# Performance work log

Measured on AMD Instinct MI355X. Metric: run time of the kernel, lower is better.

## Reference

```python
import jax, jax.numpy as jnp
import numpy as np

N_NODES = 50000
IN_F, HID_F, OUT_F = 256, 128, 40
N_EDGES = 800000


def _uniform(key, shape, scale):
    return jax.random.uniform(key, shape, dtype=jnp.float32, minval=-scale, maxval=scale)


def setup_inputs() -> dict:
    key = jax.random.key(0)
    ks = jax.random.split(key, 20)
    x = jax.random.normal(ks[0], (N_NODES, IN_F), dtype=jnp.float32)
    edge_index = jax.random.randint(ks[1], (2, N_EDGES), 0, N_NODES, dtype=jnp.int64)
    s0, sa0 = 1.0 / np.sqrt(HID_F), 1.0  # std_att = 1/sqrt(1)
    s1, sa1 = 1.0 / np.sqrt(OUT_F), 1.0
    sv = 1.0 / np.sqrt(3.0)
    return {
        "x": x, "edge_index": edge_index,
        "Wl0": _uniform(ks[2], (IN_F, HID_F), s0),
        "Wh0": _uniform(ks[3], (IN_F, HID_F), s0),
        "Wm0": _uniform(ks[4], (IN_F, HID_F), s0),
        "al0": _uniform(ks[5], (HID_F, 1), sa0),
        "ah0": _uniform(ks[6], (HID_F, 1), sa0),
        "am0": _uniform(ks[7], (HID_F, 1), sa0),
        "att0": _uniform(ks[8], (3, 3), sv),
        "Wl1": _uniform(ks[9], (HID_F, OUT_F), s1),
        "Wh1": _uniform(ks[10], (HID_F, OUT_F), s1),
        "Wm1": _uniform(ks[11], (HID_F, OUT_F), s1),
        "al1": _uniform(ks[12], (OUT_F, 1), sa1),
        "ah1": _uniform(ks[13], (OUT_F, 1), sa1),
        "am1": _uniform(ks[14], (OUT_F, 1), sa1),
        "att1": _uniform(ks[15], (3, 3), sv),
    }


def _acm_layer(x, row, col, d_inv, Wl, Wh, Wm, al, ah, am, att):
    n = x.shape[0]
    hl, hh, hm = x @ Wl, x @ Wh, x @ Wm
    # adj_low @ M  with adj_low = D^{-1}(I + A): gather sources, scatter-add to rows
    def low(M):
        return d_inv[:, None] * (M + jax.ops.segment_sum(M[col], row, num_segments=n))
    out_low = jax.nn.relu(low(hl))
    out_high = jax.nn.relu(hh - low(hh))  # adj_high = I - adj_low
    out_mlp = jax.nn.relu(hm)
    T = 3.0
    sig = jax.nn.sigmoid(jnp.concatenate([out_low @ al, out_high @ ah, out_mlp @ am], axis=1))  # [n,3]
    a = jax.nn.softmax((sig @ att) / T, axis=1)
    return 3.0 * (a[:, 0:1] * out_low + a[:, 1:2] * out_high + a[:, 2:3] * out_mlp)


def reference(x, edge_index, Wl0, Wh0, Wm0, al0, ah0, am0, att0,
              Wl1, Wh1, Wm1, al1, ah1, am1, att1):
    n = x.shape[0]
    row, col = edge_index[0], edge_index[1]
    deg = jax.ops.segment_sum(jnp.ones_like(row, dtype=jnp.float32), row, num_segments=n)
    rowsum = 1.0 + deg  # rowsum of I + A (duplicates counted, as in scipy)
    d_inv = jnp.where(rowsum > 0, 1.0 / rowsum, 0.0)
    h = _acm_layer(x, row, col, d_inv, Wl0, Wh0, Wm0, al0, ah0, am0, att0)
    out = _acm_layer(h, row, col, d_inv, Wl1, Wh1, Wm1, al1, ah1, am1, att1)
    return out
```

## Files before the change

kernel.cpp:

```cpp
#include <hip/hip_runtime.h>
#include <math.h>

#define N_NODES 50000
#define N_EDGES 800000
#define IN_F    256
#define HID_F   128
#define OUT_F   40
#define W0N     (3*HID_F)
#define W1N     (3*OUT_F)
#define NB      ((N_NODES + 255) / 256)

#define SEG     128
#define EPB     (N_EDGES / SEG)
#define NWORD   (N_NODES / 2)
#define WB      ((NWORD + 255) / 256)

#define XB   ((N_NODES * IN_F) / (256 * 16))
#define P0B  ((IN_F * W0N) / 256)
#define P1B  ((HID_F * W1N) / 256)
#define PREPB (XB + P0B + P1B)

typedef __attribute__((ext_vector_type(8))) unsigned short ushort8;
typedef __attribute__((ext_vector_type(4))) unsigned short ushort4v;
typedef __attribute__((ext_vector_type(8))) __bf16 bf16x8;
typedef __attribute__((ext_vector_type(4))) float f32x4;
typedef __attribute__((ext_vector_type(2))) float f32x2;

static __device__ __forceinline__ float sigmoidf_(float x) {
    return 1.0f / (1.0f + expf(-x));
}

static __device__ __forceinline__ unsigned short f2bf(float f) {
    unsigned u = __float_as_uint(f);
    u += 0x7FFFu + ((u >> 16) & 1u);
    return (unsigned short)(u >> 16);
}

static __device__ __forceinline__ float bflo(unsigned u) { return __uint_as_float(u << 16); }
static __device__ __forceinline__ float bfhi(unsigned u) { return __uint_as_float(u & 0xffff0000u); }


__global__ __launch_bounds__(256) void k_hist(
        const int* __restrict__ ei, unsigned* __restrict__ segHist,
        unsigned short* __restrict__ rank, unsigned* __restrict__ rc) {
    __shared__ unsigned hist[NWORD];
    int t = threadIdx.x, seg = blockIdx.x;
    for (int i = t; i < NWORD; i += 256) hist[i] = 0;
    __syncthreads();
    int base = seg * EPB;
    for (int k = t; k < EPB; k += 256) {
        int e = base + k;
        int r = ei[e];
        int c = ei[N_EDGES + e];
        unsigned old = atomicAdd(&hist[r >> 1], (r & 1) ? 0x10000u : 1u);
        unsigned lr = (r & 1) ? (old >> 16) : (old & 0xffffu);
        rank[e] = (unsigned short)lr;
        rc[e] = ((unsigned)r << 16) | (unsigned)c;
    }
    __syncthreads();
    unsigned* dst = segHist + (size_t)seg * NWORD;
    for (int i = t; i < NWORD; i += 256) dst[i] = hist[i];
}


__global__ __launch_bounds__(256) void k_scanseg(
        unsigned* __restrict__ segHist, int* __restrict__ rowPtr,
        float* __restrict__ dinv, int* __restrict__ blkTot) {
    __shared__ int s[256];
    int t = threadIdx.x;
    int w = blockIdx.x * 256 + t;
    int cum0 = 0, cum1 = 0;
    if (w < NWORD) {
        for (int sg = 0; sg < SEG; ++sg) {
            size_t idx = (size_t)sg * NWORD + w;
            unsigned h = segHist[idx];
            segHist[idx] = ((unsigned)cum1 << 16) | (unsigned)cum0;
            cum0 += (int)(h & 0xffffu);
            cum1 += (int)(h >> 16);
        }
    }
    int deg0 = cum0, deg1 = cum1;
    int pair = deg0 + deg1;
    s[t] = pair; __syncthreads();
    for (int d = 1; d < 256; d <<= 1) {
        int x = (t >= d) ? s[t - d] : 0;
        __syncthreads();
        s[t] += x;
        __syncthreads();
    }
    int basep = s[t] - pair;
    if (w < NWORD) {
        rowPtr[2 * w]     = basep;
        rowPtr[2 * w + 1] = basep + deg0;
        dinv[2 * w]     = 1.0f / (1.0f + (float)deg0);
        dinv[2 * w + 1] = 1.0f / (1.0f + (float)deg1);
    }
    if (t == 255) blkTot[blockIdx.x] = s[255];
}

__global__ void k_scan2(int* __restrict__ blk) {
    __shared__ int s[256];
    int t = threadIdx.x;
    int v = (t < WB) ? blk[t] : 0;
    s[t] = v; __syncthreads();
    for (int d = 1; d < 256; d <<= 1) {
        int x = (t >= d) ? s[t - d] : 0;
        __syncthreads();
        s[t] += x;
        __syncthreads();
    }
    if (t < WB) blk[t] = s[t] - v;
}

__global__ void k_scan3(const int* __restrict__ blkOff, int* __restrict__ rowPtr) {
    int t = threadIdx.x;
    int gid = blockIdx.x * 256 + t;
    if (gid < N_NODES) rowPtr[gid] += blkOff[gid >> 9];
    if (gid == 0) rowPtr[N_NODES] = N_EDGES;
}


__global__ __launch_bounds__(256) void k_prep(
        const float* __restrict__ x, unsigned short* __restrict__ xb,
        const float* __restrict__ Wl0, const float* __restrict__ Wh0,
        const float* __restrict__ Wm0, unsigned short* __restrict__ W0t,
        const float* __restrict__ Wl1, const float* __restrict__ Wh1,
        const float* __restrict__ Wm1, unsigned short* __restrict__ W1t) {
    int b = blockIdx.x, t = threadIdx.x;
    if (b < XB) {
        size_t idx = (size_t)b * 4096 + t * 16;
        float4 f0 = *(const float4*)(x + idx);
        float4 f1 = *(const float4*)(x + idx + 4);
        float4 f2 = *(const float4*)(x + idx + 8);
        float4 f3 = *(const float4*)(x + idx + 12);
        ushort8 u0, u1;
        u0[0]=f2bf(f0.x); u0[1]=f2bf(f0.y); u0[2]=f2bf(f0.z); u0[3]=f2bf(f0.w);
        u0[4]=f2bf(f1.x); u0[5]=f2bf(f1.y); u0[6]=f2bf(f1.z); u0[7]=f2bf(f1.w);
        u1[0]=f2bf(f2.x); u1[1]=f2bf(f2.y); u1[2]=f2bf(f2.z); u1[3]=f2bf(f2.w);
        u1[4]=f2bf(f3.x); u1[5]=f2bf(f3.y); u1[6]=f2bf(f3.z); u1[7]=f2bf(f3.w);
        *(ushort8*)(xb + idx)     = u0;
        *(ushort8*)(xb + idx + 8) = u1;
    } else if (b < XB + P0B) {
        int i = (b - XB) * 256 + t;
        int n = i / IN_F, k = i % IN_F;
        float v;
        if (n < HID_F)            v = Wl0[k * HID_F + n];
        else if (n < 2 * HID_F)   v = Wh0[k * HID_F + (n - HID_F)];
        else                      v = Wm0[k * HID_F + (n - 2 * HID_F)];
        W0t[i] = f2bf(v);
    } else {
        int i = (b - XB - P0B) * 256 + t;
        int n = i / HID_F, kp = i % HID_F;
        int k = ((kp >> 6) << 6) + ((kp & 3) << 4) + ((kp >> 2) & 15);
        float v;
        if (n < OUT_F)            v = Wl1[k * OUT_F + n];
        else if (n < 2 * OUT_F)   v = Wh1[k * OUT_F + (n - OUT_F)];
        else                      v = Wm1[k * OUT_F + (n - 2 * OUT_F)];
        W1t[i] = f2bf(v);
    }
}


#define BKP 40

template<int EPI>
__global__ __launch_bounds__(256) void k_gemm_fill(
        const unsigned short* __restrict__ A, const unsigned short* __restrict__ Bt,
        unsigned short* __restrict__ C0, int ld0,
        unsigned short* __restrict__ C1, int ld1, int nsplit,
        unsigned short* __restrict__ Hs, unsigned char* __restrict__ Hq,
        unsigned short* __restrict__ HmP,
        int M, int N, int K, int nxt,
        const unsigned* __restrict__ rc, const unsigned short* __restrict__ rank,
        const int* __restrict__ rowPtr, const unsigned short* __restrict__ segOff,
        unsigned short* __restrict__ colIdx) {
    __shared__ unsigned short As[128 * BKP];
    __shared__ unsigned short Bs[128 * BKP];
    int tid  = threadIdx.x;

    if ((int)blockIdx.x >= nxt) {
        int fid = (blockIdx.x - nxt) * gridDim.y + blockIdx.y;
        int e = fid * 256 + tid;
        if (e < N_EDGES) {
            unsigned x = rc[e];
            int r = (int)(x >> 16);
            int seg = e / EPB;
            int pos = rowPtr[r] + (int)segOff[(size_t)seg * N_NODES + r] + (int)rank[e];
            colIdx[pos] = (unsigned short)(x & 0xffffu);
        }
        return;
    }

    int lane = tid & 63, wid = tid >> 6;
    int wr = wid >> 1, wc = wid & 1;
    int bm = blockIdx.y * 128, bn = blockIdx.x * 128;

    int srow = tid >> 1;
    int scol = (tid & 1) * 16;

    int garow = min(bm + srow, M - 1);
    int gbrow = min(bn + srow, N - 1);

    f32x4 acc[4][4];
#pragma unroll
    for (int m = 0; m < 4; ++m)
#pragma unroll
        for (int n = 0; n < 4; ++n)
            acc[m][n] = (f32x4)(0.0f);

    int kg = (lane >> 4) * 8;
    int rA = wr * 64 + (lane & 15);
    int rB = wc * 64 + (lane & 15);

    for (int k0 = 0; k0 < K; k0 += 32) {
        {
            const unsigned short* src = A + (size_t)garow * K + k0 + scol;
            *(ushort8*)&As[srow * BKP + scol]     = *(const ushort8*)(src);
            *(ushort8*)&As[srow * BKP + scol + 8] = *(const ushort8*)(src + 8);
        }
        {
            const unsigned short* src = Bt + (size_t)gbrow * K + k0 + scol;
            *(ushort8*)&Bs[srow * BKP + scol]     = *(const ushort8*)(src);
            *(ushort8*)&Bs[srow * BKP + scol + 8] = *(const ushort8*)(src + 8);
        }
        __syncthreads();

        bf16x8 a[4], b[4];
#pragma unroll
        for (int m = 0; m < 4; ++m)
            a[m] = __builtin_bit_cast(bf16x8, *(const ushort8*)&As[(rA + m * 16) * BKP + kg]);
#pragma unroll
        for (int n = 0; n < 4; ++n)
            b[n] = __builtin_bit_cast(bf16x8, *(const ushort8*)&Bs[(rB + n * 16) * BKP + kg]);
#pragma unroll
        for (int m = 0; m < 4; ++m)
#pragma unroll
            for (int n = 0; n < 4; ++n)
                acc[m][n] = __builtin_amdgcn_mfma_f32_16x16x32_bf16(a[m], b[n], acc[m][n], 0, 0, 0);
        __syncthreads();
    }

    int col  = lane & 15;
    int rsub = (lane >> 4) * 4;

    if (EPI == 0) {
#pragma unroll
        for (int m = 0; m < 4; ++m) {
            int gm0 = bm + wr * 64 + m * 16 + rsub;
#pragma unroll
            for (int n = 0; n < 4; ++n) {
                int gn = bn + wc * 64 + n * 16 + col;
                if (gn >= N) continue;
#pragma unroll
                for (int j = 0; j < 4; ++j) {
                    int gm = gm0 + j;
                    if (gm >= M) continue;
                    unsigned short b = f2bf(acc[m][n][j]);
                    if (gn < nsplit) C0[(size_t)gm * ld0 + gn] = b;
                    else             C1[(size_t)gm * ld1 + (gn - nsplit)] = b;
                }
            }
        }
    } else {
#pragma unroll
        for (int m = 0; m < 4; ++m) {
            int gm0 = bm + wr * 64 + m * 16 + rsub;
#pragma unroll
            for (int j = 0; j < 4; ++j) {
                int gm = gm0 + j;
                if (gm >= M) continue;
                float v0 = acc[m][0][j], v1 = acc[m][1][j];
                float v2 = acc[m][2][j], v3 = acc[m][3][j];
                ushort4v o;
                o[0] = f2bf(v0); o[1] = f2bf(v1); o[2] = f2bf(v2); o[3] = f2bf(v3);
                if (bn < 256) {
                    int pos = bn + wc * 64 + col * 4;
                    *(ushort4v*)&Hs[(size_t)gm * 256 + pos] = o;
                    int pk = 0;
                    pk = __builtin_amdgcn_cvt_pk_fp8_f32(v0, v1, pk, false);
                    pk = __builtin_amdgcn_cvt_pk_fp8_f32(v2, v3, pk, true);
                    *(unsigned*)&Hq[(size_t)gm * 256 + pos] = (unsigned)pk;
                } else {
                    int pos = wc * 64 + col * 4;
                    *(ushort4v*)&HmP[(size_t)gm * 128 + pos] = o;
                }
            }
        }
    }
}


__global__ __launch_bounds__(256) void k_layer0(
        const unsigned short* __restrict__ Hs, const unsigned char* __restrict__ Hq,
        const unsigned short* __restrict__ HmP,
        const int* __restrict__ rowPtr, const unsigned short* __restrict__ colIdx,
        const float* __restrict__ dinv,
        const float* __restrict__ al, const float* __restrict__ ah,
        const float* __restrict__ am, const float* __restrict__ att,
        unsigned short* __restrict__ hout) {
    int lane = threadIdx.x & 63;
    int i = blockIdx.x * 4 + (threadIdx.x >> 6);

    int p0 = rowPtr[i], p1 = rowPtr[i + 1];
    float a0 = 0.f, a1 = 0.f, a2 = 0.f, a3 = 0.f;
    int off4 = lane * 4;
    int p = p0;
    for (; p + 7 < p1; p += 8) {
        int j[8];
#pragma unroll
        for (int q = 0; q < 8; ++q) j[q] = (int)colIdx[p + q];
        unsigned w[8];
#pragma unroll
        for (int q = 0; q < 8; ++q) w[q] = *(const unsigned*)(Hq + (size_t)j[q] * 256 + off4);
#pragma unroll
        for (int q = 0; q < 8; ++q) {
            f32x2 d0 = __builtin_amdgcn_cvt_pk_f32_fp8((int)w[q], false);
            f32x2 d1 = __builtin_amdgcn_cvt_pk_f32_fp8((int)w[q], true);
            a0 += d0.x; a1 += d0.y; a2 += d1.x; a3 += d1.y;
        }
    }
    for (; p < p1; ++p) {
        int j = (int)colIdx[p];
        unsigned w = *(const unsigned*)(Hq + (size_t)j * 256 + off4);
        f32x2 d0 = __builtin_amdgcn_cvt_pk_f32_fp8((int)w, false);
        f32x2 d1 = __builtin_amdgcn_cvt_pk_f32_fp8((int)w, true);
        a0 += d0.x; a1 += d0.y; a2 += d1.x; a3 += d1.y;
    }

    uint2 sv = *(const uint2*)(Hs + (size_t)i * 256 + off4);
    float s0 = bflo(sv.x), s1 = bfhi(sv.x), s2 = bflo(sv.y), s3 = bfhi(sv.y);
    float di = dinv[i];
    float l0 = di * (s0 + a0), l1 = di * (s1 + a1);
    float l2 = di * (s2 + a2), l3 = di * (s3 + a3);

    float ol0 = fmaxf(l0, 0.f), ol1 = fmaxf(l1, 0.f);
    float ol2 = fmaxf(l2, 0.f), ol3 = fmaxf(l3, 0.f);
    float oh0 = fmaxf(s0 - l0, 0.f), oh1 = fmaxf(s1 - l1, 0.f);
    float oh2 = fmaxf(s2 - l2, 0.f), oh3 = fmaxf(s3 - l3, 0.f);

    int c0 = ((lane >> 4) << 6) + (lane & 15);

    float om0 = 0.f, om1 = 0.f, om2 = 0.f, om3 = 0.f;
    float prA, prM = 0.f;
    if (lane < 32) {
        uint2 hv = *(const uint2*)(HmP + (size_t)i * 128 + off4);
        om0 = fmaxf(bflo(hv.x), 0.f); om1 = fmaxf(bfhi(hv.x), 0.f);
        om2 = fmaxf(bflo(hv.y), 0.f); om3 = fmaxf(bfhi(hv.y), 0.f);
        prA = ol0 * al[c0] + ol1 * al[c0 + 16] + ol2 * al[c0 + 32] + ol3 * al[c0 + 48];
        prM = om0 * am[c0] + om1 * am[c0 + 16] + om2 * am[c0 + 32] + om3 * am[c0 + 48];
    } else {
        int ch = c0 - 128;
        prA = oh0 * ah[ch] + oh1 * ah[ch + 16] + oh2 * ah[ch + 32] + oh3 * ah[ch + 48];
    }

#pragma unroll
    for (int d = 1; d < 32; d <<= 1) prA += __shfl_xor(prA, d);
#pragma unroll
    for (int d = 1; d < 32; d <<= 1) prM += __shfl_xor(prM, d);
    float g0 = __shfl(prA, 0);
    float g1 = __shfl(prA, 32);
    float g2 = __shfl(prM, 0);

    float sg0 = sigmoidf_(g0), sg1 = sigmoidf_(g1), sg2 = sigmoidf_(g2);
    const float inv3 = (1.0f / 3.0f);
    float e0 = (sg0 * att[0] + sg1 * att[3] + sg2 * att[6]) * inv3;
    float e1 = (sg0 * att[1] + sg1 * att[4] + sg2 * att[7]) * inv3;
    float e2 = (sg0 * att[2] + sg1 * att[5] + sg2 * att[8]) * inv3;
    float mx = fmaxf(e0, fmaxf(e1, e2));
    float x0 = expf(e0 - mx), x1 = expf(e1 - mx), x2 = expf(e2 - mx);
    float inv = 1.0f / (x0 + x1 + x2);
    float c0f = 3.0f * inv * x0, c1f = 3.0f * inv * x1, c2f = 3.0f * inv * x2;

    int src = lane | 32;
    float th0 = __shfl(oh0, src), th1 = __shfl(oh1, src);
    float th2 = __shfl(oh2, src), th3 = __shfl(oh3, src);

    if (lane < 32) {
        ushort4v o;
        o[0] = f2bf(c0f * ol0 + c1f * th0 + c2f * om0);
        o[1] = f2bf(c0f * ol1 + c1f * th1 + c2f * om1);
        o[2] = f2bf(c0f * ol2 + c1f * th2 + c2f * om2);
        o[3] = f2bf(c0f * ol3 + c1f * th3 + c2f * om3);
        *(ushort4v*)&hout[(size_t)i * 128 + off4] = o;
    }
}


__global__ __launch_bounds__(256) void k_layer1(
        const unsigned short* __restrict__ H1g, const unsigned short* __restrict__ H1m,
        const int* __restrict__ rowPtr, const unsigned short* __restrict__ colIdx,
        const float* __restrict__ dinv,
        const float* __restrict__ al, const float* __restrict__ ah,
        const float* __restrict__ am, const float* __restrict__ att,
        float* __restrict__ out) {
    int lane = threadIdx.x & 63;
    int i = blockIdx.x * 4 + (threadIdx.x >> 6);

    int p0 = rowPtr[i], p1 = rowPtr[i + 1];
    float a0 = 0.f, a1 = 0.f;
    int off = lane * 2;
    bool active = lane < 40;
    int p = p0;
    if (active) {
        for (; p + 7 < p1; p += 8) {
            int j[8];
#pragma unroll
            for (int q = 0; q < 8; ++q) j[q] = (int)colIdx[p + q];
            unsigned v[8];
#pragma unroll
            for (int q = 0; q < 8; ++q) v[q] = *(const unsigned*)(H1g + (size_t)j[q] * 80 + off);
#pragma unroll
            for (int q = 0; q < 8; ++q) { a0 += bflo(v[q]); a1 += bfhi(v[q]); }
        }
        for (; p < p1; ++p) {
            int j = (int)colIdx[p];
            unsigned v = *(const unsigned*)(H1g + (size_t)j * 80 + off);
            a0 += bflo(v); a1 += bfhi(v);
        }
    }

    float s0 = 0.f, s1 = 0.f;
    if (active) {
        unsigned sv = *(const unsigned*)(H1g + (size_t)i * 80 + off);
        s0 = bflo(sv); s1 = bfhi(sv);
    }
    float di = dinv[i];
    float l0 = di * (s0 + a0), l1 = di * (s1 + a1);

    float ol0 = fmaxf(l0, 0.f), ol1 = fmaxf(l1, 0.f);
    float oh0 = fmaxf(s0 - l0, 0.f), oh1 = fmaxf(s1 - l1, 0.f);

    float om0 = 0.f, om1 = 0.f;
    float r0 = 0.f, r1 = 0.f, r2 = 0.f;
    if (lane < 20) {
        unsigned hv = *(const unsigned*)(H1m + (size_t)i * 40 + off);
        om0 = fmaxf(bflo(hv), 0.f); om1 = fmaxf(bfhi(hv), 0.f);
        float2 alv = *(const float2*)(al + off);
        float2 amv = *(const float2*)(am + off);
        r0 = ol0 * alv.x + ol1 * alv.y;
        r2 = om0 * amv.x + om1 * amv.y;
    } else if (lane < 40) {
        float2 ahv = *(const float2*)(ah + (off - 40));
        r1 = oh0 * ahv.x + oh1 * ahv.y;
    }

#pragma unroll
    for (int d = 1; d < 64; d <<= 1) r0 += __shfl_xor(r0, d);
#pragma unroll
    for (int d = 1; d < 64; d <<= 1) r1 += __shfl_xor(r1, d);
#pragma unroll
    for (int d = 1; d < 64; d <<= 1) r2 += __shfl_xor(r2, d);

    float sg0 = sigmoidf_(r0), sg1 = sigmoidf_(r1), sg2 = sigmoidf_(r2);
    const float inv3 = (1.0f / 3.0f);
    float e0 = (sg0 * att[0] + sg1 * att[3] + sg2 * att[6]) * inv3;
    float e1 = (sg0 * att[1] + sg1 * att[4] + sg2 * att[7]) * inv3;
    float e2 = (sg0 * att[2] + sg1 * att[5] + sg2 * att[8]) * inv3;
    float mx = fmaxf(e0, fmaxf(e1, e2));
    float x0 = expf(e0 - mx), x1 = expf(e1 - mx), x2 = expf(e2 - mx);
    float inv = 1.0f / (x0 + x1 + x2);
    float c0 = 3.0f * inv * x0, c1 = 3.0f * inv * x1, c2 = 3.0f * inv * x2;

    int src = (lane + 20) & 63;
    float th0 = __shfl(oh0, src), th1 = __shfl(oh1, src);

    if (lane < 20) {
        float2 o;
        o.x = c0 * ol0 + c1 * th0 + c2 * om0;
        o.y = c0 * ol1 + c1 * th1 + c2 * om1;
        *(float2*)&out[(size_t)i * 40 + off] = o;
    }
}


extern "C" void kernel_launch(void* const* d_in, const int* in_sizes, int n_in,
                              void* d_out, int out_size, void* d_ws, size_t ws_size,
                              hipStream_t stream) {
    const float* x    = (const float*)d_in[0];
    const int*   ei   = (const int*)d_in[1];
    const float* Wl0  = (const float*)d_in[2];
    const float* Wh0  = (const float*)d_in[3];
    const float* Wm0  = (const float*)d_in[4];
    const float* al0  = (const float*)d_in[5];
    const float* ah0  = (const float*)d_in[6];
    const float* am0  = (const float*)d_in[7];
    const float* att0 = (const float*)d_in[8];
    const float* Wl1  = (const float*)d_in[9];
    const float* Wh1  = (const float*)d_in[10];
    const float* Wm1  = (const float*)d_in[11];
    const float* al1  = (const float*)d_in[12];
    const float* ah1  = (const float*)d_in[13];
    const float* am1  = (const float*)d_in[14];
    const float* att1 = (const float*)d_in[15];
    float* out = (float*)d_out;

    char* ws = (char*)d_ws;
    size_t off = 0;
    auto alloc = [&](size_t bytes) -> char* {
        char* p = ws + off;
        off += (bytes + 255) & ~(size_t)255;
        return p;
    };
    int*      rowPtr  = (int*)     alloc((size_t)(N_NODES + 1) * 4);
    int*      blkTot  = (int*)     alloc(256 * 4);
    unsigned* segHist = (unsigned*)alloc((size_t)SEG * NWORD * 4);
    unsigned short* rank   = (unsigned short*)alloc((size_t)N_EDGES * 2);
    unsigned*       rc     = (unsigned*)      alloc((size_t)N_EDGES * 4);
    unsigned short* colIdx = (unsigned short*)alloc((size_t)N_EDGES * 2);
    float* dinv   = (float*)alloc((size_t)N_NODES * 4);
    unsigned short* W0t  = (unsigned short*)alloc((size_t)W0N * IN_F * 2);
    unsigned short* W1t  = (unsigned short*)alloc((size_t)W1N * HID_F * 2);
    unsigned short* xb   = (unsigned short*)alloc((size_t)N_NODES * IN_F * 2);
    unsigned short* Hs   = (unsigned short*)alloc((size_t)N_NODES * 256 * 2);
    unsigned char*  Hq   = (unsigned char*) alloc((size_t)N_NODES * 256);
    unsigned short* HmP  = (unsigned short*)alloc((size_t)N_NODES * 128 * 2);
    unsigned short* H1g  = (unsigned short*)alloc((size_t)N_NODES * 80 * 2);
    unsigned short* H1m  = (unsigned short*)alloc((size_t)N_NODES * 40 * 2);
    unsigned short* hbuf = (unsigned short*)alloc((size_t)N_NODES * HID_F * 2);

    k_hist<<<SEG, 256, 0, stream>>>(ei, segHist, rank, rc);
    k_prep<<<PREPB, 256, 0, stream>>>(x, xb, Wl0, Wh0, Wm0, W0t,
                                      Wl1, Wh1, Wm1, W1t);
    k_scanseg<<<WB, 256, 0, stream>>>(segHist, rowPtr, dinv, blkTot);
    k_scan2<<<1, 256, 0, stream>>>(blkTot);
    k_scan3<<<NB, 256, 0, stream>>>(blkTot, rowPtr);
    {
        dim3 grid(3 + 8, (N_NODES + 127) / 128);
        k_gemm_fill<1><<<grid, 256, 0, stream>>>(xb, W0t,
                                                 nullptr, 0, nullptr, 0, 0,
                                                 Hs, Hq, HmP,
                                                 N_NODES, W0N, IN_F, 3,
                                                 rc, rank, rowPtr,
                                                 (const unsigned short*)segHist, colIdx);
    }
    k_layer0<<<N_NODES / 4, 256, 0, stream>>>(Hs, Hq, HmP, rowPtr, colIdx, dinv,
                                              al0, ah0, am0, att0, hbuf);
    {
        dim3 grid(1, (N_NODES + 127) / 128);
        k_gemm_fill<0><<<grid, 256, 0, stream>>>(hbuf, W1t,
                                                 H1g, 80, H1m, 40, 80,
                                                 nullptr, nullptr, nullptr,
                                                 N_NODES, W1N, HID_F, 1,
                                                 nullptr, nullptr, nullptr, nullptr, nullptr);
    }
    k_layer1<<<N_NODES / 4, 256, 0, stream>>>(H1g, H1m, rowPtr, colIdx, dinv,
                                              al1, ah1, am1, att1, out);
}
```

Before: 201.8 us.

## Gather layer-1 neighbors from FP8 copy and scalarize column index loads

The layer-1 GEMM epilogue now also writes an FP8 copy of the low/high features, and k_layer1 gathers neighbor rows from this 80-byte FP8 buffer with 4 features per lane instead of bf16 pairs. Both aggregation kernels load column indices as aligned 8-byte vectors and broadcast them via readfirstlane, so index loads become wave-uniform scalar values. The goal is to cut gather bandwidth and per-edge index-load overhead, at the cost of FP8 rounding in the layer-1 aggregation and extra byte-scattered stores in the GEMM epilogue.

Result: faster. 196.9 us (-2.4%).

```diff
diff --git a/kernel.cpp b/kernel.cpp
--- a/kernel.cpp
+++ b/kernel.cpp
@@ -38,6 +38,7 @@
 
 static __device__ __forceinline__ float bflo(unsigned u) { return __uint_as_float(u << 16); }
 static __device__ __forceinline__ float bfhi(unsigned u) { return __uint_as_float(u & 0xffff0000u); }
+static __device__ __forceinline__ int rfl(int v) { return __builtin_amdgcn_readfirstlane(v); }
 
 
 __global__ __launch_bounds__(256) void k_hist(
@@ -168,6 +169,7 @@
         const unsigned short* __restrict__ A, const unsigned short* __restrict__ Bt,
         unsigned short* __restrict__ C0, int ld0,
         unsigned short* __restrict__ C1, int ld1, int nsplit,
+        unsigned char* __restrict__ Cq,
         unsigned short* __restrict__ Hs, unsigned char* __restrict__ Hq,
         unsigned short* __restrict__ HmP,
         int M, int N, int K, int nxt,
@@ -255,9 +257,15 @@
                 for (int j = 0; j < 4; ++j) {
                     int gm = gm0 + j;
                     if (gm >= M) continue;
-                    unsigned short b = f2bf(acc[m][n][j]);
-                    if (gn < nsplit) C0[(size_t)gm * ld0 + gn] = b;
-                    else             C1[(size_t)gm * ld1 + (gn - nsplit)] = b;
+                    float v = acc[m][n][j];
+                    unsigned short b = f2bf(v);
+                    if (gn < nsplit) {
+                        C0[(size_t)gm * ld0 + gn] = b;
+                        int pk = __builtin_amdgcn_cvt_pk_fp8_f32(v, v, 0, false);
+                        Cq[(size_t)gm * nsplit + gn] = (unsigned char)(pk & 0xff);
+                    } else {
+                        C1[(size_t)gm * ld1 + (gn - nsplit)] = b;
+                    }
                 }
             }
         }
@@ -301,30 +309,45 @@
     int lane = threadIdx.x & 63;
     int i = blockIdx.x * 4 + (threadIdx.x >> 6);
 
-    int p0 = rowPtr[i], p1 = rowPtr[i + 1];
+    int p0 = rfl(rowPtr[i]);
+    int p1 = rfl(rowPtr[i + 1]);
     float a0 = 0.f, a1 = 0.f, a2 = 0.f, a3 = 0.f;
     int off4 = lane * 4;
-    int p = p0;
-    for (; p + 7 < p1; p += 8) {
-        int j[8];
-#pragma unroll
-        for (int q = 0; q < 8; ++q) j[q] = (int)colIdx[p + q];
-        unsigned w[8];
-#pragma unroll
-        for (int q = 0; q < 8; ++q) w[q] = *(const unsigned*)(Hq + (size_t)j[q] * 256 + off4);
-#pragma unroll
-        for (int q = 0; q < 8; ++q) {
-            f32x2 d0 = __builtin_amdgcn_cvt_pk_f32_fp8((int)w[q], false);
-            f32x2 d1 = __builtin_amdgcn_cvt_pk_f32_fp8((int)w[q], true);
-            a0 += d0.x; a1 += d0.y; a2 += d1.x; a3 += d1.y;
-        }
-    }
-    for (; p < p1; ++p) {
-        int j = (int)colIdx[p];
-        unsigned w = *(const unsigned*)(Hq + (size_t)j * 256 + off4);
+
+    auto acc1 = [&](unsigned j) {
+        const unsigned char* row = Hq + ((size_t)(j << 8));
+        unsigned w = *(const unsigned*)(row + off4);
         f32x2 d0 = __builtin_amdgcn_cvt_pk_f32_fp8((int)w, false);
         f32x2 d1 = __builtin_amdgcn_cvt_pk_f32_fp8((int)w, true);
         a0 += d0.x; a1 += d0.y; a2 += d1.x; a3 += d1.y;
+    };
+
+    int p = p0;
+    while ((p & 3) != 0 && p < p1) {
+        acc1((unsigned)rfl((int)colIdx[p]));
+        ++p;
+    }
+    for (; p + 7 < p1; p += 8) {
+        uint2 ca = *(const uint2*)(colIdx + p);
+        uint2 cb = *(const uint2*)(colIdx + p + 4);
+        unsigned w0 = (unsigned)rfl((int)ca.x);
+        unsigned w1 = (unsigned)rfl((int)ca.y);
+        unsigned w2 = (unsigned)rfl((int)cb.x);
+        unsigned w3 = (unsigned)rfl((int)cb.y);
+        acc1(w0 & 0xffffu); acc1(w0 >> 16);
+        acc1(w1 & 0xffffu); acc1(w1 >> 16);
+        acc1(w2 & 0xffffu); acc1(w2 >> 16);
+        acc1(w3 & 0xffffu); acc1(w3 >> 16);
+    }
+    for (; p + 3 < p1; p += 4) {
+        uint2 ca = *(const uint2*)(colIdx + p);
+        unsigned w0 = (unsigned)rfl((int)ca.x);
+        unsigned w1 = (unsigned)rfl((int)ca.y);
+        acc1(w0 & 0xffffu); acc1(w0 >> 16);
+        acc1(w1 & 0xffffu); acc1(w1 >> 16);
+    }
+    for (; p < p1; ++p) {
+        acc1((unsigned)rfl((int)colIdx[p]));
     }
 
     uint2 sv = *(const uint2*)(Hs + (size_t)i * 256 + off4);
@@ -387,7 +410,8 @@
 
 
 __global__ __launch_bounds__(256) void k_layer1(
-        const unsigned short* __restrict__ H1g, const unsigned short* __restrict__ H1m,
+        const unsigned short* __restrict__ H1g, const unsigned char* __restrict__ H1q,
+        const unsigned short* __restrict__ H1m,
         const int* __restrict__ rowPtr, const unsigned short* __restrict__ colIdx,
         const float* __restrict__ dinv,
         const float* __restrict__ al, const float* __restrict__ ah,
@@ -396,52 +420,77 @@
     int lane = threadIdx.x & 63;
     int i = blockIdx.x * 4 + (threadIdx.x >> 6);
 
-    int p0 = rowPtr[i], p1 = rowPtr[i + 1];
-    float a0 = 0.f, a1 = 0.f;
-    int off = lane * 2;
-    bool active = lane < 40;
-    int p = p0;
+    int p0 = rfl(rowPtr[i]);
+    int p1 = rfl(rowPtr[i + 1]);
+    float a0 = 0.f, a1 = 0.f, a2 = 0.f, a3 = 0.f;
+    int off4 = lane * 4;
+    bool active = lane < 20;
+
+    auto acc1 = [&](unsigned j) {
+        const unsigned char* row = H1q + (size_t)(j * 80u);
+        unsigned w = *(const unsigned*)(row + off4);
+        f32x2 d0 = __builtin_amdgcn_cvt_pk_f32_fp8((int)w, false);
+        f32x2 d1 = __builtin_amdgcn_cvt_pk_f32_fp8((int)w, true);
+        a0 += d0.x; a1 += d0.y; a2 += d1.x; a3 += d1.y;
+    };
+
     if (active) {
+        int p = p0;
+        while ((p & 3) != 0 && p < p1) {
+            acc1((unsigned)rfl((int)colIdx[p]));
+            ++p;
+        }
         for (; p + 7 < p1; p += 8) {
-            int j[8];
-#pragma unroll
-            for (int q = 0; q < 8; ++q) j[q] = (int)colIdx[p + q];
-            unsigned v[8];
-#pragma unroll
-            for (int q = 0; q < 8; ++q) v[q] = *(const unsigned*)(H1g + (size_t)j[q] * 80 + off);
-#pragma unroll
-            for (int q = 0; q < 8; ++q) { a0 += bflo(v[q]); a1 += bfhi(v[q]); }
+            uint2 ca = *(const uint2*)(colIdx + p);
+            uint2 cb = *(const uint2*)(colIdx + p + 4);
+            unsigned w0 = (unsigned)rfl((int)ca.x);
+            unsigned w1 = (unsigned)rfl((int)ca.y);
+            unsigned w2 = (unsigned)rfl((int)cb.x);
+            unsigned w3 = (unsigned)rfl((int)cb.y);
+            acc1(w0 & 0xffffu); acc1(w0 >> 16);
+            acc1(w1 & 0xffffu); acc1(w1 >> 16);
+            acc1(w2 & 0xffffu); acc1(w2 >> 16);
+            acc1(w3 & 0xffffu); acc1(w3 >> 16);
+        }
+        for (; p + 3 < p1; p += 4) {
+            uint2 ca = *(const uint2*)(colIdx + p);
+            unsigned w0 = (unsigned)rfl((int)ca.x);
+            unsigned w1 = (unsigned)rfl((int)ca.y);
+            acc1(w0 & 0xffffu); acc1(w0 >> 16);
+            acc1(w1 & 0xffffu); acc1(w1 >> 16);
         }
         for (; p < p1; ++p) {
-            int j = (int)colIdx[p];
-            unsigned v = *(const unsigned*)(H1g + (size_t)j * 80 + off);
-            a0 += bflo(v); a1 += bfhi(v);
-        }
-    }
-
-    float s0 = 0.f, s1 = 0.f;
+            acc1((unsigned)rfl((int)colIdx[p]));
+        }
+    }
+
+    float s0 = 0.f, s1 = 0.f, s2 = 0.f, s3 = 0.f;
     if (active) {
-        unsigned sv = *(const unsigned*)(H1g + (size_t)i * 80 + off);
-        s0 = bflo(sv); s1 = bfhi(sv);
+        uint2 sv = *(const uint2*)(H1g + (size_t)i * 80 + off4);
+        s0 = bflo(sv.x); s1 = bfhi(sv.x); s2 = bflo(sv.y); s3 = bfhi(sv.y);
     }
     float di = dinv[i];
     float l0 = di * (s0 + a0), l1 = di * (s1 + a1);
+    float l2 = di * (s2 + a2), l3 = di * (s3 + a3);
 
     float ol0 = fmaxf(l0, 0.f), ol1 = fmaxf(l1, 0.f);
+    float ol2 = fmaxf(l2, 0.f), ol3 = fmaxf(l3, 0.f);
     float oh0 = fmaxf(s0 - l0, 0.f), oh1 = fmaxf(s1 - l1, 0.f);
-
-    float om0 = 0.f, om1 = 0.f;
+    float oh2 = fmaxf(s2 - l2, 0.f), oh3 = fmaxf(s3 - l3, 0.f);
+
+    float om0 = 0.f, om1 = 0.f, om2 = 0.f, om3 = 0.f;
     float r0 = 0.f, r1 = 0.f, r2 = 0.f;
-    if (lane < 20) {
-        unsigned hv = *(const unsigned*)(H1m + (size_t)i * 40 + off);
-        om0 = fmaxf(bflo(hv), 0.f); om1 = fmaxf(bfhi(hv), 0.f);
-        float2 alv = *(const float2*)(al + off);
-        float2 amv = *(const float2*)(am + off);
-        r0 = ol0 * alv.x + ol1 * alv.y;
-        r2 = om0 * amv.x + om1 * amv.y;
-    } else if (lane < 40) {
-        float2 ahv = *(const float2*)(ah + (off - 40));
-        r1 = oh0 * ahv.x + oh1 * ahv.y;
+    if (lane < 10) {
+        uint2 hv = *(const uint2*)(H1m + (size_t)i * 40 + off4);
+        om0 = fmaxf(bflo(hv.x), 0.f); om1 = fmaxf(bfhi(hv.x), 0.f);
+        om2 = fmaxf(bflo(hv.y), 0.f); om3 = fmaxf(bfhi(hv.y), 0.f);
+        float4 alv = *(const float4*)(al + off4);
+        float4 amv = *(const float4*)(am + off4);
+        r0 = ol0 * alv.x + ol1 * alv.y + ol2 * alv.z + ol3 * alv.w;
+        r2 = om0 * amv.x + om1 * amv.y + om2 * amv.z + om3 * amv.w;
+    } else if (lane < 20) {
+        float4 ahv = *(const float4*)(ah + (off4 - 40));
+        r1 = oh0 * ahv.x + oh1 * ahv.y + oh2 * ahv.z + oh3 * ahv.w;
     }
 
 #pragma unroll
@@ -461,14 +510,17 @@
     float inv = 1.0f / (x0 + x1 + x2);
     float c0 = 3.0f * inv * x0, c1 = 3.0f * inv * x1, c2 = 3.0f * inv * x2;
 
-    int src = (lane + 20) & 63;
+    int src = (lane + 10) & 63;
     float th0 = __shfl(oh0, src), th1 = __shfl(oh1, src);
-
-    if (lane < 20) {
-        float2 o;
+    float th2 = __shfl(oh2, src), th3 = __shfl(oh3, src);
+
+    if (lane < 10) {
+        float4 o;
         o.x = c0 * ol0 + c1 * th0 + c2 * om0;
         o.y = c0 * ol1 + c1 * th1 + c2 * om1;
-        *(float2*)&out[(size_t)i * 40 + off] = o;
+        o.z = c0 * ol2 + c1 * th2 + c2 * om2;
+        o.w = c0 * ol3 + c1 * th3 + c2 * om3;
+        *(float4*)&out[(size_t)i * 40 + off4] = o;
     }
 }
 
@@ -515,6 +567,7 @@
     unsigned char*  Hq   = (unsigned char*) alloc((size_t)N_NODES * 256);
     unsigned short* HmP  = (unsigned short*)alloc((size_t)N_NODES * 128 * 2);
     unsigned short* H1g  = (unsigned short*)alloc((size_t)N_NODES * 80 * 2);
+    unsigned char*  H1q  = (unsigned char*) alloc((size_t)N_NODES * 80 + 256);
     unsigned short* H1m  = (unsigned short*)alloc((size_t)N_NODES * 40 * 2);
     unsigned short* hbuf = (unsigned short*)alloc((size_t)N_NODES * HID_F * 2);
 
@@ -527,7 +580,7 @@
     {
         dim3 grid(3 + 8, (N_NODES + 127) / 128);
         k_gemm_fill<1><<<grid, 256, 0, stream>>>(xb, W0t,
-                                                 nullptr, 0, nullptr, 0, 0,
+                                                 nullptr, 0, nullptr, 0, 0, nullptr,
                                                  Hs, Hq, HmP,
                                                  N_NODES, W0N, IN_F, 3,
                                                  rc, rank, rowPtr,
@@ -538,11 +591,11 @@
     {
         dim3 grid(1, (N_NODES + 127) / 128);
         k_gemm_fill<0><<<grid, 256, 0, stream>>>(hbuf, W1t,
-                                                 H1g, 80, H1m, 40, 80,
+                                                 H1g, 80, H1m, 40, 80, H1q,
                                                  nullptr, nullptr, nullptr,
                                                  N_NODES, W1N, HID_F, 1,
                                                  nullptr, nullptr, nullptr, nullptr, nullptr);
     }
-    k_layer1<<<N_NODES / 4, 256, 0, stream>>>(H1g, H1m, rowPtr, colIdx, dinv,
+    k_layer1<<<N_NODES / 4, 256, 0, stream>>>(H1g, H1q, H1m, rowPtr, colIdx, dinv,
                                               al1, ah1, am1, att1, out);
 }
```
